# Performance work log

Measured on AMD Instinct MI355X. Metric: run time of the kernel, lower is better.

The kernel has to match this reference:

```python
import jax, jax.numpy as jnp
import numpy as np

LAYERS = [2048, 2048, 2048, 512]
THRESHOLD = 1.0
TAU_MEM = 20.0
TAU_SYN = 5.0
DT = 1.0
BATCH = 32
T = 100


def setup_inputs() -> dict:
    key = jax.random.key(0)
    ks = jax.random.split(key, 2 + 2 * (len(LAYERS) - 1))
    inp = {
        "x": jax.random.uniform(ks[0], (BATCH, LAYERS[0]), dtype=jnp.float32),
        "noise": jax.random.uniform(ks[1], (T, BATCH, LAYERS[0]), dtype=jnp.float32),
        "time_steps": T,
    }
    # nn.Linear-style init: U(-1/sqrt(fan_in), 1/sqrt(fan_in))
    for i in range(len(LAYERS) - 1):
        fan_in, fan_out = LAYERS[i], LAYERS[i + 1]
        bound = 1.0 / np.sqrt(fan_in)
        inp[f"W{i}"] = jax.random.uniform(ks[2 + 2 * i], (fan_out, fan_in), minval=-bound, maxval=bound, dtype=jnp.float32)
        inp[f"b{i}"] = jax.random.uniform(ks[3 + 2 * i], (fan_out,), minval=-bound, maxval=bound, dtype=jnp.float32)
    return inp


def _lif_step(I, mem, syn):
    # dI_syn/dt = -I_syn/tau_syn + I ; dV/dt = -V/tau_mem + I_syn  (explicit Euler, dt=1)
    syn = syn + (-syn / TAU_SYN + I) * DT
    mem = mem + (-mem / TAU_MEM + syn) * DT
    spikes = (mem >= THRESHOLD).astype(mem.dtype)
    mem = mem * (1.0 - spikes)          # reset fired neurons
    mem = mem * (mem > 0).astype(mem.dtype)  # clamp negative potentials to 0
    return spikes, mem, syn


def reference(x, noise, W0, b0, W1, b1, W2, b2, time_steps):
    params = [(W0, b0), (W1, b1), (W2, b2)]
    batch = x.shape[0]
    dtype = x.dtype
    rate = jnp.clip(x, 0.0, 1.0)                       # [B, in]
    in_spikes = (noise < rate[None]).astype(dtype)     # [T, B, in] Poisson encoding

    mems = tuple(jnp.zeros((batch, W.shape[0]), dtype) for W, _ in params)
    syns = tuple(jnp.zeros((batch, W.shape[0]), dtype) for W, _ in params)

    def step(carry, sp_in):
        mems, syns = carry
        layer_in = sp_in
        new_mems, new_syns = [], []
        count = jnp.zeros((), dtype)
        for (W, b), m, s in zip(params, mems, syns):
            I = layer_in @ W.T + b
            spk, m, s = _lif_step(I, m, s)
            new_mems.append(m)
            new_syns.append(s)
            count = count + spk.sum()
            layer_in = spk
        return (tuple(new_mems), tuple(new_syns)), (layer_in, count)

    (_, _), (out_spikes, counts) = jax.lax.scan(step, (mems, syns), in_spikes)
    output = out_spikes.mean(axis=0)   # [B, out]: time-averaged output spike train
    total_spikes = counts.sum()
    return output, total_spikes
```

## Files before the change

### kernel.cpp

```cpp
#include <hip/hip_runtime.h>

#define T_STEPS 100
#define MTOT    3200
#define R0_OFF  0
#define R1_OFF  13107200
#define I_OFF   26214400

typedef _Float16 half8_t __attribute__((ext_vector_type(8)));
typedef _Float16 half4_t __attribute__((ext_vector_type(4)));
typedef float    f32x4   __attribute__((ext_vector_type(4)));

__device__ __forceinline__ void encode_body(
    int blk, const float* __restrict__ x, const float* __restrict__ noise,
    _Float16* __restrict__ spk0, float* __restrict__ out)
{
    if (blk == 0 && threadIdx.x == 0) out[16384] = 0.0f;
    const int tid = threadIdx.x;
    const int m0  = blk * 16;
    __shared__ half8_t lds[16 * 257];
    #pragma unroll
    for (int ml = 0; ml < 16; ++ml) {
        const int m = m0 + ml;
        const int t = m >> 5, b = m & 31;
        const float4 x1 = *(const float4*)(x + b * 2048 + tid * 8);
        const float4 x2 = *(const float4*)(x + b * 2048 + tid * 8 + 4);
        const float4 n1 = *(const float4*)(noise + (size_t)t * 65536 + b * 2048 + tid * 8);
        const float4 n2 = *(const float4*)(noise + (size_t)t * 65536 + b * 2048 + tid * 8 + 4);
        const float xr[8] = {x1.x,x1.y,x1.z,x1.w,x2.x,x2.y,x2.z,x2.w};
        const float nz[8] = {n1.x,n1.y,n1.z,n1.w,n2.x,n2.y,n2.z,n2.w};
        half8_t sp;
        #pragma unroll
        for (int j = 0; j < 8; ++j) {
            const float r = fminf(fmaxf(xr[j], 0.0f), 1.0f);
            sp[j] = (nz[j] < r) ? (_Float16)1.0f : (_Float16)0.0f;
        }
        lds[ml * 257 + tid] = sp;
    }
    __syncthreads();
    #pragma unroll
    for (int r = 0; r < 16; ++r) {
        const int ml  = tid & 15;
        const int oct = r * 16 + (tid >> 4);
        *(half8_t*)(spk0 + ((size_t)oct * MTOT + m0 + ml) * 8) = lds[ml * 257 + oct];
    }
}

__device__ __forceinline__ void convw_body(
    int blk, const float* __restrict__ W, _Float16* __restrict__ Wf)
{
    const int koct = threadIdx.x;
    #pragma unroll
    for (int r = 0; r < 8; ++r) {
        const int row = blk * 8 + r;
        const float* wp = W + (size_t)row * 2048 + koct * 8;
        const float4 f1 = *(const float4*)(wp);
        const float4 f2 = *(const float4*)(wp + 4);
        half8_t h = {(_Float16)f1.x,(_Float16)f1.y,(_Float16)f1.z,(_Float16)f1.w,
                     (_Float16)f2.x,(_Float16)f2.y,(_Float16)f2.z,(_Float16)f2.w};
        const size_t idx = (size_t)(row >> 4) * 32768
                         + ((size_t)((koct >> 2) * 64 + (koct & 3) * 16 + (row & 15))) * 8;
        *(half8_t*)(Wf + idx) = h;
    }
}

__device__ __forceinline__ void scan_body(
    int blk, const _Float16* __restrict__ I, const float* __restrict__ bias,
    _Float16* __restrict__ spk_out, float* __restrict__ out,
    const int nshift, const int is_last)
{
    const int gid = blk * 256 + threadIdx.x;
    const int N = 1 << nshift;
    const int n = gid & (N - 1);
    const int b = gid >> nshift;
    const float bi = bias[n];
    const size_t nbase = (size_t)(n >> 3) * (MTOT * 8) + (n & 7);
    float mem = 0.f, syn = 0.f, osum = 0.f, cnt = 0.f;
    #pragma unroll 4
    for (int t = 0; t < T_STEPS; ++t) {
        const int m = t * 32 + b;
        const float Iv = (float)I[nbase + (size_t)m * 8] + bi;
        syn = syn + (-syn / 5.0f + Iv);
        mem = mem + (-mem / 20.0f + syn);
        const float sv = (mem >= 1.0f) ? 1.0f : 0.0f;
        mem = (sv != 0.0f) ? 0.0f : mem;
        mem = (mem > 0.0f) ? mem : 0.0f;
        cnt += sv; osum += sv;
        if (!is_last) spk_out[nbase + (size_t)m * 8] = (_Float16)sv;
    }
    if (is_last) out[b * 512 + n] = osum * 0.01f;
    float c = cnt;
    #pragma unroll
    for (int s2 = 1; s2 < 64; s2 <<= 1) c += __shfl_xor(c, s2);
    if ((threadIdx.x & 63) == 0) atomicAdd(&out[16384], c);
}

__global__ __launch_bounds__(256, 2) void snn_enc_convw_kernel(
    const float* __restrict__ x, const float* __restrict__ noise,
    _Float16* __restrict__ spk0, float* __restrict__ out,
    const float* __restrict__ W, _Float16* __restrict__ Wf)
{
    if (blockIdx.x < 200) encode_body(blockIdx.x, x, noise, spk0, out);
    else                  convw_body(blockIdx.x - 200, W, Wf);
}

__global__ __launch_bounds__(256, 4) void snn_scan_convw_kernel(
    const _Float16* __restrict__ I, const float* __restrict__ bias,
    _Float16* __restrict__ spk_out, float* __restrict__ out,
    const int scan_blocks, const int nshift,
    const float* __restrict__ W, _Float16* __restrict__ Wf)
{
    if ((int)blockIdx.x < scan_blocks)
        scan_body(blockIdx.x, I, bias, spk_out, out, nshift, 0);
    else
        convw_body(blockIdx.x - scan_blocks, W, Wf);
}

__global__ __launch_bounds__(256, 4) void snn_scan_kernel(
    const _Float16* __restrict__ I, const float* __restrict__ bias,
    float* __restrict__ out, const int nshift)
{
    scan_body(blockIdx.x, I, bias, nullptr, out, nshift, 1);
}

template<int NC, int TPW>
__global__ __launch_bounds__(1024, 4) void snn_gemm_kernel(
    const _Float16* __restrict__ Wf, const _Float16* __restrict__ spk,
    _Float16* __restrict__ I)
{
    const int tid  = threadIdx.x;
    const int lane = tid & 63;
    const int w    = tid >> 6;
    const int quad = lane >> 4, mi = lane & 15;
    const int chunk = blockIdx.x % NC;
    const int nbb   = blockIdx.x / NC;
    const int row_base = nbb * 32;
    const int jcount = (200 - chunk + NC - 1) / NC;

    __shared__ _Float16 wlds[32 * 2048];
    {
        const half8_t* __restrict__ src = (const half8_t*)(Wf + (size_t)nbb * 65536);
        half8_t* __restrict__ dst = (half8_t*)wlds;
        #pragma unroll
        for (int r = 0; r < 8; ++r) dst[tid + r * 1024] = src[tid + r * 1024];
    }
    __syncthreads();

    for (int jl0 = TPW * w; jl0 < jcount; jl0 += 16 * TPW) {
        int mt[TPW]; bool val[TPW];
        const _Float16* bp[TPW];
        #pragma unroll
        for (int u = 0; u < TPW; ++u) {
            const int jl = jl0 + u;
            val[u] = jl < jcount;
            mt[u]  = chunk + NC * (val[u] ? jl : jl0);
            bp[u]  = spk + ((size_t)mt[u] * 16 + mi) * 8;
        }
        f32x4 acc[TPW][2];
        #pragma unroll
        for (int u = 0; u < TPW; ++u) { acc[u][0] = (f32x4){0,0,0,0}; acc[u][1] = (f32x4){0,0,0,0}; }

        half8_t bc[TPW];
        const size_t k0 = (size_t)quad * (MTOT * 8);
        #pragma unroll
        for (int u = 0; u < TPW; ++u) bc[u] = *(const half8_t*)(bp[u] + k0);

        #pragma unroll 4
        for (int kb = 0; kb < 64; ++kb) {
            half8_t bn[TPW];
            if (kb < 63) {
                const size_t kn = (size_t)((kb + 1) * 4 + quad) * (MTOT * 8);
                #pragma unroll
                for (int u = 0; u < TPW; ++u) bn[u] = *(const half8_t*)(bp[u] + kn);
            }
            const half8_t a0 = *(const half8_t*)(wlds + ((size_t)(kb * 64 + lane)) * 8);
            const half8_t a1 = *(const half8_t*)(wlds + 32768 + ((size_t)(kb * 64 + lane)) * 8);
            #pragma unroll
            for (int u = 0; u < TPW; ++u) {
                acc[u][0] = __builtin_amdgcn_mfma_f32_16x16x32_f16(a0, bc[u], acc[u][0], 0, 0, 0);
                acc[u][1] = __builtin_amdgcn_mfma_f32_16x16x32_f16(a1, bc[u], acc[u][1], 0, 0, 0);
            }
            #pragma unroll
            for (int u = 0; u < TPW; ++u) bc[u] = bn[u];
        }
        #pragma unroll
        for (int s = 0; s < 2; ++s) {
            const int n0 = row_base + s * 16 + quad * 4;
            const size_t obase = (size_t)(n0 >> 3) * (MTOT * 8) + (n0 & 7);
            #pragma unroll
            for (int u = 0; u < TPW; ++u) {
                if (!val[u]) continue;
                half4_t h;
                #pragma unroll
                for (int r = 0; r < 4; ++r) h[r] = (_Float16)acc[u][s][r];
                *(half4_t*)(I + obase + (size_t)(mt[u] * 16 + mi) * 8) = h;
            }
        }
    }
}

extern "C" void kernel_launch(void* const* d_in, const int* in_sizes, int n_in,
                              void* d_out, int out_size, void* d_ws, size_t ws_size,
                              hipStream_t stream) {
    const float* x     = (const float*)d_in[0];
    const float* noise = (const float*)d_in[1];
    const float* W0 = (const float*)d_in[3];
    const float* b0 = (const float*)d_in[4];
    const float* W1 = (const float*)d_in[5];
    const float* b1 = (const float*)d_in[6];
    const float* W2 = (const float*)d_in[7];
    const float* b2 = (const float*)d_in[8];
    float* out = (float*)d_out;

    _Float16* R0 = (_Float16*)((char*)d_ws + R0_OFF);
    _Float16* R1 = (_Float16*)((char*)d_ws + R1_OFF);
    _Float16* Ib = (_Float16*)((char*)d_ws + I_OFF);

    snn_enc_convw_kernel<<<dim3(456), dim3(256), 0, stream>>>(x, noise, R0, out, W0, R1);
    snn_gemm_kernel<4, 4><<<dim3(256), dim3(1024), 0, stream>>>(R1, R0, Ib);
    snn_scan_convw_kernel<<<dim3(512), dim3(256), 0, stream>>>(Ib, b0, R1, out, 256, 11, W1, R0);
    snn_gemm_kernel<4, 4><<<dim3(256), dim3(1024), 0, stream>>>(R0, R1, Ib);
    snn_scan_convw_kernel<<<dim3(320), dim3(256), 0, stream>>>(Ib, b1, R0, out, 256, 11, W2, R1);
    snn_gemm_kernel<16, 1><<<dim3(256), dim3(1024), 0, stream>>>(R1, R0, Ib);
    snn_scan_kernel<<<dim3(64), dim3(256), 0, stream>>>(Ib, b2, out, 9);

    (void)in_sizes; (void)n_in; (void)out_size; (void)ws_size;
}
```

Before: 290.4 us.

## Add 64-row GEMM kernel with K-staged LDS weights for 2048-wide layers

Replaces the 32-row, 1024-thread GEMM for the two 2048x2048 layers with a 512-thread kernel that covers 64 output rows per block. It stages the weight tile into LDS in four K-quarters using direct global-to-LDS loads and prefetches the B operand two k-steps ahead. The M tiles are split across 16 blocks per row group, with some waves handling two M tiles. The aim is better reuse of each weight fragment across M and lower LDS footprint per block. The cost is synchronisation between stages and uneven per-wave work.

```diff
diff --git a/kernel.cpp b/kernel.cpp
--- a/kernel.cpp
+++ b/kernel.cpp
@@ -122,6 +122,139 @@
     scan_body(blockIdx.x, I, bias, nullptr, out, nshift, 1);
 }
 
+
+__device__ __forceinline__ half8_t ldB(const _Float16* __restrict__ p, int kq) {
+    return *(const half8_t*)(p + (size_t)kq * (MTOT * 8));
+}
+
+__device__ __forceinline__ void stage_q(
+    const _Float16* __restrict__ Wf, _Float16* __restrict__ wlds,
+    const int nbb, const int q, const int w, const int lane)
+{
+    #pragma unroll
+    for (int r = 0; r < 8; ++r) {
+        const int unit = r * 512 + w * 64 + lane;
+        const int s = unit >> 10, off = unit & 1023;
+        const _Float16* src = Wf + (size_t)(4 * nbb + s) * 32768
+                            + (size_t)q * 8192 + (size_t)off * 8;
+        _Float16* dst = wlds + (size_t)unit * 8;
+        __builtin_amdgcn_global_load_lds(
+            (const __attribute__((address_space(1))) void*)src,
+            (__attribute__((address_space(3))) void*)dst, 16, 0, 0);
+    }
+}
+
+template<bool HAS2>
+__device__ __forceinline__ void kstep512(
+    const _Float16* __restrict__ wlds, const _Float16* const (&bp)[2],
+    half8_t (&bb)[2], f32x4 (&acc)[2][4],
+    const int lane, const int quad, const int kb, const int j)
+{
+    half8_t a[4];
+    #pragma unroll
+    for (int s = 0; s < 4; ++s)
+        a[s] = *(const half8_t*)(wlds + (size_t)s * 8192 + (size_t)(j * 64 + lane) * 8);
+    #pragma unroll
+    for (int s = 0; s < 4; ++s) {
+        acc[0][s] = __builtin_amdgcn_mfma_f32_16x16x32_f16(a[s], bb[0], acc[0][s], 0, 0, 0);
+        if (HAS2)
+            acc[1][s] = __builtin_amdgcn_mfma_f32_16x16x32_f16(a[s], bb[1], acc[1][s], 0, 0, 0);
+    }
+    if (kb + 2 < 64) {
+        const int kq = (kb + 2) * 4 + quad;
+        bb[0] = ldB(bp[0], kq);
+        if (HAS2) bb[1] = ldB(bp[1], kq);
+    }
+}
+
+template<bool HAS2>
+__device__ __forceinline__ void gemm64s_run(
+    const _Float16* __restrict__ Wf, const _Float16* __restrict__ spk,
+    _Float16* __restrict__ I, _Float16* __restrict__ wlds,
+    const int (&mt)[2], const int nbb, const int row_base,
+    const int w, const int lane, const int quad, const int mi)
+{
+    const _Float16* bp[2];
+    bp[0] = spk + ((size_t)mt[0] * 16 + mi) * 8;
+    bp[1] = spk + ((size_t)mt[1] * 16 + mi) * 8;
+
+    half8_t bE[2], bO[2];
+    bE[0] = ldB(bp[0], quad);
+    bO[0] = ldB(bp[0], 4 + quad);
+    if (HAS2) { bE[1] = ldB(bp[1], quad); bO[1] = ldB(bp[1], 4 + quad); }
+
+    stage_q(Wf, wlds, nbb, 0, w, lane);
+    __syncthreads();
+
+    f32x4 acc[2][4];
+    #pragma unroll
+    for (int u = 0; u < 2; ++u) {
+        #pragma unroll
+        for (int s = 0; s < 4; ++s) acc[u][s] = (f32x4){0, 0, 0, 0};
+    }
+
+    #pragma unroll 1
+    for (int q = 0; q < 4; ++q) {
+        #pragma unroll
+        for (int j = 0; j < 16; j += 2) {
+            kstep512<HAS2>(wlds, bp, bE, acc, lane, quad, q * 16 + j,     j);
+            kstep512<HAS2>(wlds, bp, bO, acc, lane, quad, q * 16 + j + 1, j + 1);
+        }
+        __syncthreads();
+        if (q < 3) {
+            stage_q(Wf, wlds, nbb, q + 1, w, lane);
+            __syncthreads();
+        }
+    }
+
+    #pragma unroll
+    for (int s = 0; s < 4; ++s) {
+        const int n0 = row_base + s * 16 + quad * 4;
+        const size_t obase = (size_t)(n0 >> 3) * (MTOT * 8) + (n0 & 7);
+        #pragma unroll
+        for (int u = 0; u < 2; ++u) {
+            if (u == 1 && !HAS2) continue;
+            half4_t h;
+            #pragma unroll
+            for (int r = 0; r < 4; ++r) h[r] = (_Float16)acc[u][s][r];
+            *(half4_t*)(I + obase + (size_t)(mt[u] * 16 + mi) * 8) = h;
+        }
+    }
+}
+
+__global__ __launch_bounds__(512, 4) void snn_gemm64s_kernel(
+    const _Float16* __restrict__ Wf, const _Float16* __restrict__ spk,
+    _Float16* __restrict__ I)
+{
+    const int tid  = threadIdx.x;
+    const int lane = tid & 63;
+    const int w    = tid >> 6;
+    const int mi   = lane & 15;
+    const int quad = lane >> 4;
+    const int chunk = blockIdx.x & 7;
+    const int msl   = (blockIdx.x >> 3) & 1;
+    const int nbb   = blockIdx.x >> 4;
+    const int row_base = nbb * 64;
+    const int jbase  = msl ? 13 : 0;
+    const int jcount = msl ? 12 : 13;
+    const int rem    = jcount - 8;
+    const bool has2  = (w < rem);
+    const int jl_start = jbase + (has2 ? 2 * w : w + rem);
+
+    int mt[2];
+    #pragma unroll
+    for (int u = 0; u < 2; ++u) {
+        int jl = jl_start + u;
+        if (jl >= jbase + jcount) jl = jbase + jcount - 1;
+        mt[u] = chunk + 8 * jl;
+    }
+
+    __shared__ _Float16 wlds[32768];
+
+    if (has2) gemm64s_run<true >(Wf, spk, I, wlds, mt, nbb, row_base, w, lane, quad, mi);
+    else      gemm64s_run<false>(Wf, spk, I, wlds, mt, nbb, row_base, w, lane, quad, mi);
+}
+
 template<int NC, int TPW>
 __global__ __launch_bounds__(1024, 4) void snn_gemm_kernel(
     const _Float16* __restrict__ Wf, const _Float16* __restrict__ spk,
@@ -216,9 +349,9 @@
     _Float16* Ib = (_Float16*)((char*)d_ws + I_OFF);
 
     snn_enc_convw_kernel<<<dim3(456), dim3(256), 0, stream>>>(x, noise, R0, out, W0, R1);
-    snn_gemm_kernel<4, 4><<<dim3(256), dim3(1024), 0, stream>>>(R1, R0, Ib);
+    snn_gemm64s_kernel<<<dim3(512), dim3(512), 0, stream>>>(R1, R0, Ib);
     snn_scan_convw_kernel<<<dim3(512), dim3(256), 0, stream>>>(Ib, b0, R1, out, 256, 11, W1, R0);
-    snn_gemm_kernel<4, 4><<<dim3(256), dim3(1024), 0, stream>>>(R0, R1, Ib);
+    snn_gemm64s_kernel<<<dim3(512), dim3(512), 0, stream>>>(R0, R1, Ib);
     snn_scan_convw_kernel<<<dim3(320), dim3(256), 0, stream>>>(Ib, b1, R0, out, 256, 11, W2, R1);
     snn_gemm_kernel<16, 1><<<dim3(256), dim3(1024), 0, stream>>>(R1, R0, Ib);
     snn_scan_kernel<<<dim3(64), dim3(256), 0, stream>>>(Ib, b2, out, 9);
```

Measured after the change: 274.8 us. -5.4%, faster.
